# Kernel optimization log

Hardware: AMD Instinct MI355X
Metric: run time of the kernel (lower is better)

Reference implementation:

```python
import jax, jax.numpy as jnp
import numpy as np

AX = (-2, -1)
LAMBDA = 0.05
ITERS = 6

# torch fft_2d_img  = fftshift(ifft2(ifftshift(x)))  (used in the FORWARD model)
# torch ifft_2d_img = ifftshift(fft2(fftshift(x)))   (used in the ADJOINT model)

def _fwd_xform(x):
    return jnp.fft.fftshift(jnp.fft.ifft2(jnp.fft.ifftshift(x, axes=AX), axes=AX, norm='ortho'), axes=AX)

def _adj_xform(x):
    return jnp.fft.ifftshift(jnp.fft.fft2(jnp.fft.fftshift(x, axes=AX), axes=AX, norm='ortho'), axes=AX)

def _forward_model(img, S, mask):
    # img [b,t,h,w] -> masked multicoil k-space [b,t,c,h,w]
    return mask * _fwd_xform(S * img[:, :, None])

def _adjoint_model(k, S):
    # k [b,t,c,h,w] -> coil-combined image [b,t,h,w]
    return jnp.sum(jnp.conj(S) * _adj_xform(k), axis=2)

def _system_matrix_R(p, S, L, mask):
    # p [b,sv,h,w]; L [b,t,sv]
    expanded = jnp.einsum('bts,bshw->bthw', L, p)
    combined = _adjoint_model(_forward_model(expanded, S, mask), S)
    out = jnp.einsum('bts,bthw->bshw', jnp.conj(L), combined)
    return out + LAMBDA * p

def _cg_solve(b_vec, S, L, mask):
    z0 = jnp.zeros_like(b_vec)
    rs0 = jnp.vdot(b_vec, b_vec)

    def step(carry, _):
        z, r, p, rs_old, done = carry
        Ap = _system_matrix_R(p, S, L, mask)
        alpha = rs_old / (jnp.vdot(p, Ap) + 1e-20)
        z_n = z + alpha * p
        r_n = r - alpha * Ap
        rs_new = jnp.vdot(r_n, r_n)
        p_n = r_n + (rs_new / (rs_old + 1e-20)) * p
        # replicate torch early-break: freeze state once residual is tiny
        z_o = jnp.where(done, z, z_n)
        r_o = jnp.where(done, r, r_n)
        p_o = jnp.where(done, p, p_n)
        rs_o = jnp.where(done, rs_old, rs_new)
        done_n = done | (jnp.abs(rs_o) < 1e-10)
        return (z_o, r_o, p_o, rs_o, done_n), None

    carry0 = (z0, b_vec, b_vec, rs0, jnp.array(False))
    (z, _, _, _, _), _ = jax.lax.scan(step, carry0, None, length=ITERS)
    return z

def setup_inputs() -> dict:
    key = jax.random.key(0)
    ks = jax.random.split(key, 9)
    b, t, c, h, w, sv = 2, 12, 10, 256, 256, 3
    f32 = jnp.float32
    inp = {
        'k_real': jax.random.normal(ks[0], (b, t, c, h, w), f32),
        'k_imag': jax.random.normal(ks[1], (b, t, c, h, w), f32),
        'mo_real': jax.random.normal(ks[2], (b, sv, h, w), f32),
        'mo_imag': jax.random.normal(ks[3], (b, sv, h, w), f32),
        's_real': jax.random.normal(ks[4], (b, 1, c, h, w), f32),
        's_imag': jax.random.normal(ks[5], (b, 1, c, h, w), f32),
        'tb_real': jax.random.normal(ks[6], (b, t, sv), f32),
        'tb_imag': jax.random.normal(ks[7], (b, t, sv), f32),
        'mask': (jax.random.uniform(ks[8], (b, t, 1, h, w)) < 0.35).astype(f32),
    }
    return inp

def reference(k_real, k_imag, mo_real, mo_imag, s_real, s_imag, tb_real, tb_imag, mask):
    Y = k_real + 1j * k_imag          # [b,t,c,h,w]
    MO = mo_real + 1j * mo_imag       # [b,sv,h,w]
    S = s_real + 1j * s_imag          # [b,1,c,h,w]
    L = tb_real + 1j * tb_imag        # [b,t,sv]
    # b = L^H A^H Y + lambda * model_output
    b_vec = jnp.einsum('bts,bthw->bshw', jnp.conj(L), _adjoint_model(Y, S)) + LAMBDA * MO
    z = _cg_solve(b_vec, S, L, mask)  # [b,sv,h,w] complex
    return jnp.stack([z.real, z.imag], axis=-1)  # [b,sv,h,w,2] float32
```

## Files before the change

### kernel.cpp

```cpp
#include <hip/hip_runtime.h>
#include <math.h>

#define HW 65536
#define LAM 0.05f

struct Scal {
  double pap_re, pap_im, rq_re, rq_im, qq;
  double rs_old, al_re, al_im, beta;
  int done, apply, cnt, pad;
};

__device__ __forceinline__ float2 cadd(float2 a, float2 b){ return make_float2(a.x+b.x, a.y+b.y); }
__device__ __forceinline__ float2 csub(float2 a, float2 b){ return make_float2(a.x-b.x, a.y-b.y); }
__device__ __forceinline__ float2 cmul(float2 a, float2 b){
  return make_float2(a.x*b.x - a.y*b.y, a.x*b.y + a.y*b.x);
}
__device__ __forceinline__ float2 cmulj(float2 a, float2 b){
  return make_float2(a.x*b.x + a.y*b.y, a.x*b.y - a.y*b.x);
}
__device__ __forceinline__ int swz(int p){ return p ^ (p>>4); }

__device__ __forceinline__ void wave_lds_sync(){
  __builtin_amdgcn_wave_barrier();
  __asm__ __volatile__("s_waitcnt lgkmcnt(0)" ::: "memory");
  __builtin_amdgcn_wave_barrier();
}

template<int S>
__device__ __forceinline__ void bfly4(float2 x0, float2 x1, float2 x2, float2 x3,
                                      float2& y0, float2& y1, float2& y2, float2& y3){
  float2 a  = cadd(x0,x2), bm = csub(x0,x2);
  float2 c  = cadd(x1,x3), d  = csub(x1,x3);
  float2 jd = make_float2(-(float)S*d.y, (float)S*d.x);
  y0 = cadd(a,c); y2 = csub(a,c); y1 = cadd(bm,jd); y3 = csub(bm,jd);
}

template<int S>
__device__ __forceinline__ void dft16(float2* a){
  const float s_ = (float)S;
  const float2 W1 = make_float2( 0.92387953251f,  s_*0.38268343236f);
  const float2 W2 = make_float2( 0.70710678119f,  s_*0.70710678119f);
  const float2 W3 = make_float2( 0.38268343236f,  s_*0.92387953251f);
  const float2 W4_ = make_float2(0.f,              s_*1.f);
  const float2 W6 = make_float2(-0.70710678119f,  s_*0.70710678119f);
  const float2 W9 = make_float2(-0.92387953251f, -s_*0.38268343236f);
  float2 t[16];
#pragma unroll
  for (int n0=0;n0<4;n0++){
    float2 y0,y1,y2,y3;
    bfly4<S>(a[n0], a[n0+4], a[n0+8], a[n0+12], y0,y1,y2,y3);
    if (n0==1){ y1=cmul(y1,W1); y2=cmul(y2,W2); y3=cmul(y3,W3); }
    if (n0==2){ y1=cmul(y1,W2); y2=cmul(y2,W4_); y3=cmul(y3,W6); }
    if (n0==3){ y1=cmul(y1,W3); y2=cmul(y2,W6); y3=cmul(y3,W9); }
    t[n0*4+0]=y0; t[n0*4+1]=y1; t[n0*4+2]=y2; t[n0*4+3]=y3;
  }
#pragma unroll
  for (int k1=0;k1<4;k1++){
    float2 y0,y1,y2,y3;
    bfly4<S>(t[0*4+k1], t[1*4+k1], t[2*4+k1], t[3*4+k1], y0,y1,y2,y3);
    a[k1+0]=y0; a[k1+4]=y1; a[k1+8]=y2; a[k1+12]=y3;
  }
}

template<int S>
__device__ void fft256_r16(float2* buf, int l){
  float2 a[16];
#pragma unroll
  for (int j=0;j<16;j++) a[j] = buf[swz(l + 16*j)];
  dft16<S>(a);
  float ang = (float)S * 6.2831853071795865f * (float)l * (1.f/256.f);
  float sn, cs; __sincosf(ang, &sn, &cs);
  float2 wstep = make_float2(cs, sn);
  float2 w = wstep;
#pragma unroll
  for (int k=1;k<16;k++){ a[k] = cmul(a[k], w); w = cmul(w, wstep); }
#pragma unroll
  for (int k=0;k<16;k++) buf[swz(16*k + l)] = a[k];
  wave_lds_sync();
#pragma unroll
  for (int j=0;j<16;j++) a[j] = buf[swz(16*l + j)];
  dft16<S>(a);
  wave_lds_sync();
#pragma unroll
  for (int k=0;k<16;k++) buf[swz(l + 16*k)] = a[k];
  wave_lds_sync();
}

__global__ __launch_bounds__(256) void k_w(const float* __restrict__ mask,
                                           const float* __restrict__ tbr,
                                           const float* __restrict__ tbi,
                                           float* __restrict__ Wf,
                                           Scal* sc){
  if (blockIdx.x==0 && blockIdx.y==0 && threadIdx.x==0){
    sc->pap_re=0.0; sc->pap_im=0.0; sc->rq_re=0.0; sc->rq_im=0.0; sc->qq=0.0;
    sc->rs_old=0.0; sc->al_re=0.0; sc->al_im=0.0; sc->beta=0.0;
    sc->done=0; sc->apply=0; sc->cnt=0;
  }
  __shared__ float wtf[9][16][17];
  int tid = threadIdx.x;
  int bx = blockIdx.x;
  int b  = blockIdx.y;
  int u0 = (bx>>4)<<4, v0 = (bx&15)<<4;
  int u_l = tid>>4, v_l = tid&15;
  int pix = (u0+u_l)*256 + (v0+v_l);
  float d0=0,d1=0,d2=0, o01r=0,o01i=0, o02r=0,o02i=0, o12r=0,o12i=0;
#pragma unroll
  for (int t=0;t<12;t++){
    float m = mask[(size_t)(b*12+t)*HW + pix];
    int lb = (b*12+t)*3;
    float l0r = tbr[lb+0], l0i = tbi[lb+0];
    float l1r = tbr[lb+1], l1i = tbi[lb+1];
    float l2r = tbr[lb+2], l2i = tbi[lb+2];
    d0 += m*(l0r*l0r + l0i*l0i);
    d1 += m*(l1r*l1r + l1i*l1i);
    d2 += m*(l2r*l2r + l2i*l2i);
    o01r += m*(l0r*l1r + l0i*l1i); o01i += m*(l0r*l1i - l0i*l1r);
    o02r += m*(l0r*l2r + l0i*l2i); o02i += m*(l0r*l2i - l0i*l2r);
    o12r += m*(l1r*l2r + l1i*l2i); o12i += m*(l1r*l2i - l1i*l2r);
  }
  const float s = 1.0f/65536.0f;
  wtf[0][u_l][v_l] = d0*s;   wtf[1][u_l][v_l] = d1*s;   wtf[2][u_l][v_l] = d2*s;
  wtf[3][u_l][v_l] = o01r*s; wtf[4][u_l][v_l] = o01i*s;
  wtf[5][u_l][v_l] = o02r*s; wtf[6][u_l][v_l] = o02i*s;
  wtf[7][u_l][v_l] = o12r*s; wtf[8][u_l][v_l] = o12i*s;
  __syncthreads();
  int u_l2 = tid&15, v_l2 = tid>>4;
#pragma unroll
  for (int f=0;f<9;f++){
    Wf[ ((size_t)(b*9+f)*256 + (v0+v_l2))*256 + (u0+u_l2) ] = wtf[f][u_l2][v_l2];
  }
}

__global__ __launch_bounds__(512) void k_yrow(const float* __restrict__ kr,
                                              const float* __restrict__ ki,
                                              const float* __restrict__ tbr,
                                              const float* __restrict__ tbi,
                                              float2* __restrict__ bufA){
  __shared__ float2 lb[30*257];
  int tid = threadIdx.x;
  int wv = tid>>6, lane = tid&63, g = lane>>4, l = lane&15;
  int px = tid & 255, half = tid >> 8;
  int r = blockIdx.x, b = blockIdx.y;
  float sg = (((r ^ px) & 1) ? -1.f : 1.f) * (1.f/256.f);
  int sk = swz(px);
#pragma unroll
  for (int cc=0; cc<5; cc++){
    int c = half*5 + cc;
    float a0r=0,a0i=0,a1r=0,a1i=0,a2r=0,a2i=0;
#pragma unroll
    for (int t=0;t<12;t++){
      size_t off = ((size_t)((b*12+t)*10+c))*HW + (size_t)r*256 + px;
      float yr = kr[off], yi = ki[off];
      int lbi = (b*12+t)*3;
      float l0r = tbr[lbi+0], l0i = tbi[lbi+0];
      float l1r = tbr[lbi+1], l1i = tbi[lbi+1];
      float l2r = tbr[lbi+2], l2i = tbi[lbi+2];
      a0r += l0r*yr + l0i*yi;  a0i += l0r*yi - l0i*yr;
      a1r += l1r*yr + l1i*yi;  a1i += l1r*yi - l1i*yr;
      a2r += l2r*yr + l2i*yi;  a2i += l2r*yi - l2i*yr;
    }
    lb[(c*3+0)*257 + sk] = make_float2(a0r*sg, a0i*sg);
    lb[(c*3+1)*257 + sk] = make_float2(a1r*sg, a1i*sg);
    lb[(c*3+2)*257 + sk] = make_float2(a2r*sg, a2i*sg);
  }
  __syncthreads();
  int tau = 4*wv + g;
  if (tau < 30){
    float2* lw = &lb[tau*257];
    fft256_r16<-1>(lw, l);
    float2* dst = bufA + (size_t)(b*30+tau)*HW + (size_t)r*256;
#pragma unroll
    for (int j=0;j<8;j++){
      int e = 2*(16*j + l);
      float2 e0 = lw[swz(e)], e1 = lw[swz(e+1)];
      *(float4*)(dst + e) = make_float4(e0.x,e0.y,e1.x,e1.y);
    }
  }
}

template<int MODE>
__global__ __launch_bounds__(384) void k_colpass(float2* __restrict__ bufA,
                                                 const float* __restrict__ Wf){
  __shared__ float2 lb[24*257];
  int tid = threadIdx.x;
  int wv = tid>>6, lane = tid&63, g = lane>>4, l = lane&15;
  int j0 = blockIdx.x*8;
  int c = blockIdx.y, b = blockIdx.z;
#pragma unroll
  for (int it=0; it<8; it++){
    int idx = it*384 + tid;
    int s = idx>>10, rem = idx&1023, u = rem>>2, cp = rem&3;
    const float2* src = bufA + (size_t)(b*30 + c*3 + s)*HW;
    float4 v = *(const float4*)(src + u*256 + j0 + 2*cp);
    lb[(s*8+2*cp  )*257 + swz(u)] = make_float2(v.x, v.y);
    lb[(s*8+2*cp+1)*257 + swz(u)] = make_float2(v.z, v.w);
  }
  __syncthreads();
  int tau = 4*wv + g;
  if (MODE==0){
    fft256_r16<-1>(&lb[tau*257], l);
  } else {
    fft256_r16<1>(&lb[tau*257], l);
    __syncthreads();
    const float* W0 = Wf + (size_t)b*9*HW;
    for (int idx=tid; idx<2048; idx+=384){
      int u = idx&255, col = idx>>8;
      int su = swz(u);
      int v = j0 + col;
      float2 x0 = lb[(0*8+col)*257 + su];
      float2 x1 = lb[(1*8+col)*257 + su];
      float2 x2 = lb[(2*8+col)*257 + su];
      size_t wb = (size_t)v*256 + u;
      float d0  = W0[(size_t)0*HW + wb];
      float d1  = W0[(size_t)1*HW + wb];
      float d2  = W0[(size_t)2*HW + wb];
      float o01r= W0[(size_t)3*HW + wb], o01i = W0[(size_t)4*HW + wb];
      float o02r= W0[(size_t)5*HW + wb], o02i = W0[(size_t)6*HW + wb];
      float o12r= W0[(size_t)7*HW + wb], o12i = W0[(size_t)8*HW + wb];
      float2 y0, y1, y2;
      y0.x = d0*x0.x + o01r*x1.x - o01i*x1.y + o02r*x2.x - o02i*x2.y;
      y0.y = d0*x0.y + o01r*x1.y + o01i*x1.x + o02r*x2.y + o02i*x2.x;
      y1.x = o01r*x0.x + o01i*x0.y + d1*x1.x + o12r*x2.x - o12i*x2.y;
      y1.y = o01r*x0.y - o01i*x0.x + d1*x1.y + o12r*x2.y + o12i*x2.x;
      y2.x = o02r*x0.x + o02i*x0.y + o12r*x1.x + o12i*x1.y + d2*x2.x;
      y2.y = o02r*x0.y - o02i*x0.x + o12r*x1.y - o12i*x1.x + d2*x2.y;
      lb[(0*8+col)*257 + su] = y0;
      lb[(1*8+col)*257 + su] = y1;
      lb[(2*8+col)*257 + su] = y2;
    }
    __syncthreads();
    fft256_r16<-1>(&lb[tau*257], l);
  }
  __syncthreads();
#pragma unroll
  for (int it=0; it<8; it++){
    int idx = it*384 + tid;
    int s = idx>>10, rem = idx&1023, u = rem>>2, cp = rem&3;
    float2* dst = bufA + (size_t)(b*30 + c*3 + s)*HW;
    float2 e0 = lb[(s*8+2*cp  )*257 + swz(u)];
    float2 e1 = lb[(s*8+2*cp+1)*257 + swz(u)];
    *(float4*)(dst + u*256 + j0 + 2*cp) = make_float4(e0.x, e0.y, e1.x, e1.y);
  }
}

__global__ __launch_bounds__(256) void k_combine(const float2* __restrict__ bufA,
                                                 const float* __restrict__ sr_,
                                                 const float* __restrict__ si_,
                                                 const float* __restrict__ mor,
                                                 const float* __restrict__ moi,
                                                 float2* __restrict__ z,
                                                 float2* __restrict__ r,
                                                 float2* __restrict__ p,
                                                 Scal* sc){
  __shared__ double sd[4];
  int tid = threadIdx.x;
  int i = blockIdx.x*256 + tid;
  int pix = i & (HW-1);
  int bs = i >> 16;
  int b = bs/3, s = bs - 3*b;
  float2 acc = make_float2(0.f, 0.f);
#pragma unroll
  for (int c=0;c<10;c++){
    float2 F  = bufA[(size_t)(b*30 + c*3 + s)*HW + pix];
    size_t so = (size_t)(b*10+c)*HW + pix;
    float2 sv = make_float2(sr_[so], si_[so]);
    acc = cadd(acc, cmulj(sv, F));
  }
  float sgl = (((pix>>8)^pix)&1 ? -1.f : 1.f) * LAM;
  acc.x += sgl*mor[i]; acc.y += sgl*moi[i];
  z[i] = make_float2(0.f,0.f);
  r[i] = acc; p[i] = acc;
  double dre = (double)acc.x*acc.x + (double)acc.y*acc.y;
  for (int off=32; off>0; off>>=1) dre += __shfl_down(dre, off, 64);
  if ((tid&63)==0) sd[tid>>6] = dre;
  __syncthreads();
  if (tid==0) atomicAdd(&sc->rs_old, sd[0]+sd[1]+sd[2]+sd[3]);
}

__global__ __launch_bounds__(512) void k_spfft(float2* __restrict__ p,
                                               float2* __restrict__ rvec,
                                               float2* __restrict__ z,
                                               const float2* __restrict__ Ap,
                                               const float* __restrict__ sr_,
                                               const float* __restrict__ si_,
                                               float2* __restrict__ bufA,
                                               Scal* sc){
  __shared__ float2 lb[30*257];
  int tid = threadIdx.x;
  int wv = tid>>6, lane = tid&63, g = lane>>4, l = lane&15;
  int r = blockIdx.x, b = blockIdx.y;
  if (tid < 256){
    int px = tid, sk = swz(px);
    int ap = sc->apply;
    float2 alpha = make_float2((float)sc->al_re, (float)sc->al_im);
    float beta = (float)sc->beta;
    float2 pv[3];
#pragma unroll
    for (int s=0;s<3;s++){
      size_t oi = (size_t)(b*3+s)*HW + (size_t)r*256 + px;
      float2 pvv = p[oi];
      if (ap){
        float2 zv = z[oi], rv = rvec[oi], apv = Ap[oi];
        zv = cadd(zv, cmul(alpha, pvv));
        rv = csub(rv, cmul(alpha, apv));
        float2 pn = make_float2(rv.x + beta*pvv.x, rv.y + beta*pvv.y);
        z[oi] = zv; rvec[oi] = rv; p[oi] = pn;
        pvv = pn;
      }
      pv[s] = pvv;
    }
#pragma unroll
    for (int c=0;c<10;c++){
      size_t so = (size_t)(b*10+c)*HW + (size_t)r*256 + px;
      float2 sv = make_float2(sr_[so], si_[so]);
      lb[(c*3+0)*257 + sk] = cmul(sv, pv[0]);
      lb[(c*3+1)*257 + sk] = cmul(sv, pv[1]);
      lb[(c*3+2)*257 + sk] = cmul(sv, pv[2]);
    }
  }
  __syncthreads();
  int tau = 4*wv + g;
  if (tau < 30){
    float2* lw = &lb[tau*257];
    fft256_r16<1>(lw, l);
    float2* dst = bufA + (size_t)(b*30+tau)*HW + (size_t)r*256;
#pragma unroll
    for (int j=0;j<8;j++){
      int e = 2*(16*j + l);
      float2 e0 = lw[swz(e)], e1 = lw[swz(e+1)];
      *(float4*)(dst + e) = make_float4(e0.x,e0.y,e1.x,e1.y);
    }
  }
}

__global__ __launch_bounds__(512) void k_rowcomb(const float2* __restrict__ bufA,
                                                 const float* __restrict__ sr_,
                                                 const float* __restrict__ si_,
                                                 const float2* __restrict__ pvec,
                                                 const float2* __restrict__ rvec,
                                                 float2* __restrict__ Ap,
                                                 Scal* sc){
  __shared__ float2 lb[30*257];
  __shared__ double sd[5][8];
  int tid = threadIdx.x;
  int wv = tid>>6, lane = tid&63, g = lane>>4, l = lane&15;
  int r = blockIdx.x, b = blockIdx.y;
  int tau = 4*wv + g;
  if (tau < 30){
    const float2* src = bufA + (size_t)(b*30+tau)*HW + (size_t)r*256;
    float2* lw = &lb[tau*257];
#pragma unroll
    for (int j=0;j<8;j++){
      int e = 2*(16*j + l);
      float4 v = *(const float4*)(src + e);
      lw[swz(e)]   = make_float2(v.x, v.y);
      lw[swz(e+1)] = make_float2(v.z, v.w);
    }
    wave_lds_sync();
    fft256_r16<-1>(lw, l);
  }
  __syncthreads();
  double d0=0.0, d1=0.0, d2=0.0, d3=0.0, d4=0.0;
  if (tid < 256){
    int px = tid, sk = swz(px);
    float2 a0={0,0}, a1={0,0}, a2={0,0};
#pragma unroll
    for (int c=0;c<10;c++){
      size_t so = (size_t)(b*10+c)*HW + (size_t)r*256 + px;
      float2 sv = make_float2(sr_[so], si_[so]);
      a0 = cadd(a0, cmulj(sv, lb[(c*3+0)*257 + sk]));
      a1 = cadd(a1, cmulj(sv, lb[(c*3+1)*257 + sk]));
      a2 = cadd(a2, cmulj(sv, lb[(c*3+2)*257 + sk]));
    }
    float2 accs[3] = {a0,a1,a2};
#pragma unroll
    for (int s=0;s<3;s++){
      size_t oi = (size_t)(b*3+s)*HW + (size_t)r*256 + px;
      float2 acc = accs[s];
      float2 av = pvec[oi];
      float2 rv = rvec[oi];
      acc.x += LAM*av.x; acc.y += LAM*av.y;
      Ap[oi] = acc;
      d0 += (double)av.x*acc.x + (double)av.y*acc.y;
      d1 += (double)av.x*acc.y - (double)av.y*acc.x;
      d2 += (double)rv.x*acc.x + (double)rv.y*acc.y;
      d3 += (double)rv.x*acc.y - (double)rv.y*acc.x;
      d4 += (double)acc.x*acc.x + (double)acc.y*acc.y;
    }
  }
  for (int off=32; off>0; off>>=1){
    d0 += __shfl_down(d0, off, 64);
    d1 += __shfl_down(d1, off, 64);
    d2 += __shfl_down(d2, off, 64);
    d3 += __shfl_down(d3, off, 64);
    d4 += __shfl_down(d4, off, 64);
  }
  if (lane==0){ sd[0][wv]=d0; sd[1][wv]=d1; sd[2][wv]=d2; sd[3][wv]=d3; sd[4][wv]=d4; }
  __syncthreads();
  if (tid==0){
    double t0=0,t1=0,t2=0,t3=0,t4=0;
#pragma unroll
    for (int q=0;q<8;q++){ t0+=sd[0][q]; t1+=sd[1][q]; t2+=sd[2][q]; t3+=sd[3][q]; t4+=sd[4][q]; }
    atomicAdd(&sc->pap_re, t0); atomicAdd(&sc->pap_im, t1);
    atomicAdd(&sc->rq_re,  t2); atomicAdd(&sc->rq_im,  t3);
    atomicAdd(&sc->qq,     t4);
    int total = (int)(gridDim.x*gridDim.y);
    int prev = atomicAdd(&sc->cnt, 1);
    if (prev == total-1){
      sc->cnt = 0;
      if (!sc->done){
        double pr = sc->pap_re + 1e-20, pi = sc->pap_im;
        double den = pr*pr + pi*pi;
        double rs = sc->rs_old;
        double alr =  rs*pr/den, ali = -rs*pi/den;
        double rs_new = rs - 2.0*(alr*sc->rq_re - ali*sc->rq_im)
                           + (alr*alr + ali*ali)*sc->qq;
        sc->al_re = alr; sc->al_im = ali;
        sc->beta = rs_new/(rs + 1e-20);
        sc->rs_old = rs_new;
        sc->apply = 1;
        if (fabs(rs_new) < 1e-10) sc->done = 1;
      } else {
        sc->apply = 0;
      }
      sc->pap_re=0.0; sc->pap_im=0.0; sc->rq_re=0.0; sc->rq_im=0.0; sc->qq=0.0;
    }
  }
}

__global__ __launch_bounds__(256) void k_out(const float2* __restrict__ z,
                                             const float2* __restrict__ p,
                                             const Scal* sc,
                                             float* __restrict__ out){
  int i = blockIdx.x*256 + threadIdx.x;
  int pix = i & (HW-1);
  float sgn = (((pix>>8)^pix)&1) ? -1.f : 1.f;
  float2 zv = z[i];
  if (sc->apply){
    float2 alpha = make_float2((float)sc->al_re, (float)sc->al_im);
    zv = cadd(zv, cmul(alpha, p[i]));
  }
  out[2*i]   = sgn*zv.x;
  out[2*i+1] = sgn*zv.y;
}

extern "C" void kernel_launch(void* const* d_in, const int* in_sizes, int n_in,
                              void* d_out, int out_size, void* d_ws, size_t ws_size,
                              hipStream_t stream){
  const float* kr   = (const float*)d_in[0];
  const float* ki   = (const float*)d_in[1];
  const float* mor  = (const float*)d_in[2];
  const float* moi  = (const float*)d_in[3];
  const float* sr   = (const float*)d_in[4];
  const float* si   = (const float*)d_in[5];
  const float* tbr  = (const float*)d_in[6];
  const float* tbi  = (const float*)d_in[7];
  const float* mask = (const float*)d_in[8];
  float* out = (float*)d_out;

  float2* ws   = (float2*)d_ws;
  float2* bufA = ws;
  float*  Wf   = (float*)(ws + 3932160);
  float2* z    = ws + 4521984;
  float2* r    = ws + 4915200;
  float2* p    = ws + 5308416;
  float2* Ap   = ws + 5701632;
  Scal*   sc   = (Scal*)(ws + 6094848);

  k_w<<<dim3(256,2),dim3(256),0,stream>>>(mask, tbr, tbi, Wf, sc);
  k_yrow<<<dim3(256,2),dim3(512),0,stream>>>(kr, ki, tbr, tbi, bufA);
  k_colpass<0><<<dim3(32,10,2),dim3(384),0,stream>>>(bufA, Wf);
  k_combine<<<dim3(1536),dim3(256),0,stream>>>(bufA, sr, si, mor, moi,
                                               z, r, p, sc);
  for (int it=0; it<6; ++it){
    k_spfft<<<dim3(256,2),dim3(512),0,stream>>>(p, r, z, Ap, sr, si, bufA, sc);
    k_colpass<1><<<dim3(32,10,2),dim3(384),0,stream>>>(bufA, Wf);
    k_rowcomb<<<dim3(256,2),dim3(512),0,stream>>>(bufA, sr, si, p, r, Ap, sc);
  }
  k_out<<<dim3(1536),dim3(256),0,stream>>>(z, p, sc, out);
}
```

Baseline: 725.6 us.

## Vectorize loads, interleave weight layout, and spread coil work across all threads

k_yrow now runs 640 threads, one wave per coil, each lane loading float4 of k-space for four pixels. The nine per-pixel weight planes are interleaved into two float4 planes plus one scalar plane, so colpass reads three loads instead of nine. k_spfft and k_rowcomb now use all 512 threads for the coil loops: the p update is staged through shared memory, and the coil sum is split into two halves that are reduced through LDS. The aim is wider memory transactions and less idle half-block time, at the cost of extra LDS traffic and barriers.

```diff
diff --git a/kernel.cpp b/kernel.cpp
--- a/kernel.cpp
+++ b/kernel.cpp
@@ -125,45 +125,64 @@
   wtf[7][u_l][v_l] = o12r*s; wtf[8][u_l][v_l] = o12i*s;
   __syncthreads();
   int u_l2 = tid&15, v_l2 = tid>>4;
-#pragma unroll
-  for (int f=0;f<9;f++){
-    Wf[ ((size_t)(b*9+f)*256 + (v0+v_l2))*256 + (u0+u_l2) ] = wtf[f][u_l2][v_l2];
-  }
-}
-
-__global__ __launch_bounds__(512) void k_yrow(const float* __restrict__ kr,
-                                              const float* __restrict__ ki,
-                                              const float* __restrict__ tbr,
-                                              const float* __restrict__ tbi,
-                                              float2* __restrict__ bufA){
+  float* W0 = Wf + (size_t)b*9*HW;
+  float4* WA = (float4*)W0;
+  float4* WB = (float4*)(W0 + (size_t)4*HW);
+  float*  WC = W0 + (size_t)8*HW;
+  size_t wb = (size_t)(v0+v_l2)*256 + (u0+u_l2);
+  WA[wb] = make_float4(wtf[0][u_l2][v_l2], wtf[1][u_l2][v_l2],
+                       wtf[2][u_l2][v_l2], wtf[3][u_l2][v_l2]);
+  WB[wb] = make_float4(wtf[4][u_l2][v_l2], wtf[5][u_l2][v_l2],
+                       wtf[6][u_l2][v_l2], wtf[7][u_l2][v_l2]);
+  WC[wb] = wtf[8][u_l2][v_l2];
+}
+
+__global__ __launch_bounds__(640,5) void k_yrow(const float* __restrict__ kr,
+                                                const float* __restrict__ ki,
+                                                const float* __restrict__ tbr,
+                                                const float* __restrict__ tbi,
+                                                float2* __restrict__ bufA){
   __shared__ float2 lb[30*257];
   int tid = threadIdx.x;
-  int wv = tid>>6, lane = tid&63, g = lane>>4, l = lane&15;
-  int px = tid & 255, half = tid >> 8;
   int r = blockIdx.x, b = blockIdx.y;
-  float sg = (((r ^ px) & 1) ? -1.f : 1.f) * (1.f/256.f);
-  int sk = swz(px);
-#pragma unroll
-  for (int cc=0; cc<5; cc++){
-    int c = half*5 + cc;
-    float a0r=0,a0i=0,a1r=0,a1i=0,a2r=0,a2i=0;
+  {
+    int c = tid>>6, px4 = tid&63;
+    float ar[3][4], ai[3][4];
+#pragma unroll
+    for (int s=0;s<3;s++)
+#pragma unroll
+      for (int j=0;j<4;j++){ ar[s][j]=0.f; ai[s][j]=0.f; }
 #pragma unroll
     for (int t=0;t<12;t++){
-      size_t off = ((size_t)((b*12+t)*10+c))*HW + (size_t)r*256 + px;
-      float yr = kr[off], yi = ki[off];
+      size_t off = ((size_t)((b*12+t)*10+c))*HW + (size_t)r*256 + 4*px4;
+      float4 yr4 = *(const float4*)(kr + off);
+      float4 yi4 = *(const float4*)(ki + off);
       int lbi = (b*12+t)*3;
       float l0r = tbr[lbi+0], l0i = tbi[lbi+0];
       float l1r = tbr[lbi+1], l1i = tbi[lbi+1];
       float l2r = tbr[lbi+2], l2i = tbi[lbi+2];
-      a0r += l0r*yr + l0i*yi;  a0i += l0r*yi - l0i*yr;
-      a1r += l1r*yr + l1i*yi;  a1i += l1r*yi - l1i*yr;
-      a2r += l2r*yr + l2i*yi;  a2i += l2r*yi - l2i*yr;
-    }
-    lb[(c*3+0)*257 + sk] = make_float2(a0r*sg, a0i*sg);
-    lb[(c*3+1)*257 + sk] = make_float2(a1r*sg, a1i*sg);
-    lb[(c*3+2)*257 + sk] = make_float2(a2r*sg, a2i*sg);
-  }
-  __syncthreads();
+      float yrj[4] = {yr4.x, yr4.y, yr4.z, yr4.w};
+      float yij[4] = {yi4.x, yi4.y, yi4.z, yi4.w};
+#pragma unroll
+      for (int j=0;j<4;j++){
+        float yr = yrj[j], yi = yij[j];
+        ar[0][j] += l0r*yr + l0i*yi;  ai[0][j] += l0r*yi - l0i*yr;
+        ar[1][j] += l1r*yr + l1i*yi;  ai[1][j] += l1r*yi - l1i*yr;
+        ar[2][j] += l2r*yr + l2i*yi;  ai[2][j] += l2r*yi - l2i*yr;
+      }
+    }
+#pragma unroll
+    for (int j=0;j<4;j++){
+      int px = 4*px4 + j;
+      float sg = (((r ^ px) & 1) ? -1.f : 1.f) * (1.f/256.f);
+      int sk = swz(px);
+#pragma unroll
+      for (int s=0;s<3;s++)
+        lb[(c*3+s)*257 + sk] = make_float2(ar[s][j]*sg, ai[s][j]*sg);
+    }
+  }
+  __syncthreads();
+  int wv = tid>>6, lane = tid&63, g = lane>>4, l = lane&15;
   int tau = 4*wv + g;
   if (tau < 30){
     float2* lw = &lb[tau*257];
@@ -203,6 +222,9 @@
     fft256_r16<1>(&lb[tau*257], l);
     __syncthreads();
     const float* W0 = Wf + (size_t)b*9*HW;
+    const float4* WA = (const float4*)W0;
+    const float4* WB = (const float4*)(W0 + (size_t)4*HW);
+    const float*  WC = W0 + (size_t)8*HW;
     for (int idx=tid; idx<2048; idx+=384){
       int u = idx&255, col = idx>>8;
       int su = swz(u);
@@ -211,12 +233,11 @@
       float2 x1 = lb[(1*8+col)*257 + su];
       float2 x2 = lb[(2*8+col)*257 + su];
       size_t wb = (size_t)v*256 + u;
-      float d0  = W0[(size_t)0*HW + wb];
-      float d1  = W0[(size_t)1*HW + wb];
-      float d2  = W0[(size_t)2*HW + wb];
-      float o01r= W0[(size_t)3*HW + wb], o01i = W0[(size_t)4*HW + wb];
-      float o02r= W0[(size_t)5*HW + wb], o02i = W0[(size_t)6*HW + wb];
-      float o12r= W0[(size_t)7*HW + wb], o12i = W0[(size_t)8*HW + wb];
+      float4 wa = WA[wb];
+      float4 wbv = WB[wb];
+      float d0 = wa.x, d1 = wa.y, d2 = wa.z, o01r = wa.w;
+      float o01i = wbv.x, o02r = wbv.y, o02i = wbv.z, o12r = wbv.w;
+      float o12i = WC[wb];
       float2 y0, y1, y2;
       y0.x = d0*x0.x + o01r*x1.x - o01i*x1.y + o02r*x2.x - o02i*x2.y;
       y0.y = d0*x0.y + o01r*x1.y + o01i*x1.x + o02r*x2.y + o02i*x2.x;
@@ -286,36 +307,39 @@
                                                float2* __restrict__ bufA,
                                                Scal* sc){
   __shared__ float2 lb[30*257];
+  __shared__ float2 pbuf[3][256];
   int tid = threadIdx.x;
   int wv = tid>>6, lane = tid&63, g = lane>>4, l = lane&15;
   int r = blockIdx.x, b = blockIdx.y;
-  if (tid < 256){
-    int px = tid, sk = swz(px);
-    int ap = sc->apply;
-    float2 alpha = make_float2((float)sc->al_re, (float)sc->al_im);
-    float beta = (float)sc->beta;
-    float2 pv[3];
-#pragma unroll
-    for (int s=0;s<3;s++){
-      size_t oi = (size_t)(b*3+s)*HW + (size_t)r*256 + px;
-      float2 pvv = p[oi];
-      if (ap){
-        float2 zv = z[oi], rv = rvec[oi], apv = Ap[oi];
-        zv = cadd(zv, cmul(alpha, pvv));
-        rv = csub(rv, cmul(alpha, apv));
-        float2 pn = make_float2(rv.x + beta*pvv.x, rv.y + beta*pvv.y);
-        z[oi] = zv; rvec[oi] = rv; p[oi] = pn;
-        pvv = pn;
-      }
-      pv[s] = pvv;
-    }
-#pragma unroll
-    for (int c=0;c<10;c++){
+  int ap = sc->apply;
+  float2 alpha = make_float2((float)sc->al_re, (float)sc->al_im);
+  float beta = (float)sc->beta;
+  for (int i = tid; i < 768; i += 512){
+    int s = i>>8, px = i&255;
+    size_t oi = (size_t)(b*3+s)*HW + (size_t)r*256 + px;
+    float2 pvv = p[oi];
+    if (ap){
+      float2 zv = z[oi], rv = rvec[oi], apv = Ap[oi];
+      zv = cadd(zv, cmul(alpha, pvv));
+      rv = csub(rv, cmul(alpha, apv));
+      float2 pn = make_float2(rv.x + beta*pvv.x, rv.y + beta*pvv.y);
+      z[oi] = zv; rvec[oi] = rv; p[oi] = pn;
+      pvv = pn;
+    }
+    pbuf[s][px] = pvv;
+  }
+  __syncthreads();
+  {
+    int px = tid & 255, h = tid >> 8, sk = swz(px);
+    float2 pv0 = pbuf[0][px], pv1 = pbuf[1][px], pv2 = pbuf[2][px];
+#pragma unroll
+    for (int k=0;k<5;k++){
+      int c = h + 2*k;
       size_t so = (size_t)(b*10+c)*HW + (size_t)r*256 + px;
       float2 sv = make_float2(sr_[so], si_[so]);
-      lb[(c*3+0)*257 + sk] = cmul(sv, pv[0]);
-      lb[(c*3+1)*257 + sk] = cmul(sv, pv[1]);
-      lb[(c*3+2)*257 + sk] = cmul(sv, pv[2]);
+      lb[(c*3+0)*257 + sk] = cmul(sv, pv0);
+      lb[(c*3+1)*257 + sk] = cmul(sv, pv1);
+      lb[(c*3+2)*257 + sk] = cmul(sv, pv2);
     }
   }
   __syncthreads();
@@ -341,7 +365,8 @@
                                                  float2* __restrict__ Ap,
                                                  Scal* sc){
   __shared__ float2 lb[30*257];
-  __shared__ double sd[5][8];
+  __shared__ float2 part[3][256];
+  __shared__ double sd[5][4];
   int tid = threadIdx.x;
   int wv = tid>>6, lane = tid&63, g = lane>>4, l = lane&15;
   int r = blockIdx.x, b = blockIdx.y;
@@ -360,18 +385,24 @@
     fft256_r16<-1>(lw, l);
   }
   __syncthreads();
+  int px = tid & 255, h = tid >> 8, sk = swz(px);
+  float2 a0={0,0}, a1={0,0}, a2={0,0};
+#pragma unroll
+  for (int k=0;k<5;k++){
+    int c = h + 2*k;
+    size_t so = (size_t)(b*10+c)*HW + (size_t)r*256 + px;
+    float2 sv = make_float2(sr_[so], si_[so]);
+    a0 = cadd(a0, cmulj(sv, lb[(c*3+0)*257 + sk]));
+    a1 = cadd(a1, cmulj(sv, lb[(c*3+1)*257 + sk]));
+    a2 = cadd(a2, cmulj(sv, lb[(c*3+2)*257 + sk]));
+  }
+  if (h==1){ part[0][px]=a0; part[1][px]=a1; part[2][px]=a2; }
+  __syncthreads();
   double d0=0.0, d1=0.0, d2=0.0, d3=0.0, d4=0.0;
   if (tid < 256){
-    int px = tid, sk = swz(px);
-    float2 a0={0,0}, a1={0,0}, a2={0,0};
-#pragma unroll
-    for (int c=0;c<10;c++){
-      size_t so = (size_t)(b*10+c)*HW + (size_t)r*256 + px;
-      float2 sv = make_float2(sr_[so], si_[so]);
-      a0 = cadd(a0, cmulj(sv, lb[(c*3+0)*257 + sk]));
-      a1 = cadd(a1, cmulj(sv, lb[(c*3+1)*257 + sk]));
-      a2 = cadd(a2, cmulj(sv, lb[(c*3+2)*257 + sk]));
-    }
+    a0 = cadd(a0, part[0][px]);
+    a1 = cadd(a1, part[1][px]);
+    a2 = cadd(a2, part[2][px]);
     float2 accs[3] = {a0,a1,a2};
 #pragma unroll
     for (int s=0;s<3;s++){
@@ -395,12 +426,12 @@
     d3 += __shfl_down(d3, off, 64);
     d4 += __shfl_down(d4, off, 64);
   }
-  if (lane==0){ sd[0][wv]=d0; sd[1][wv]=d1; sd[2][wv]=d2; sd[3][wv]=d3; sd[4][wv]=d4; }
+  if (lane==0 && wv<4){ sd[0][wv]=d0; sd[1][wv]=d1; sd[2][wv]=d2; sd[3][wv]=d3; sd[4][wv]=d4; }
   __syncthreads();
   if (tid==0){
     double t0=0,t1=0,t2=0,t3=0,t4=0;
 #pragma unroll
-    for (int q=0;q<8;q++){ t0+=sd[0][q]; t1+=sd[1][q]; t2+=sd[2][q]; t3+=sd[3][q]; t4+=sd[4][q]; }
+    for (int q=0;q<4;q++){ t0+=sd[0][q]; t1+=sd[1][q]; t2+=sd[2][q]; t3+=sd[3][q]; t4+=sd[4][q]; }
     atomicAdd(&sc->pap_re, t0); atomicAdd(&sc->pap_im, t1);
     atomicAdd(&sc->rq_re,  t2); atomicAdd(&sc->rq_im,  t3);
     atomicAdd(&sc->qq,     t4);
@@ -468,7 +499,7 @@
   Scal*   sc   = (Scal*)(ws + 6094848);
 
   k_w<<<dim3(256,2),dim3(256),0,stream>>>(mask, tbr, tbi, Wf, sc);
-  k_yrow<<<dim3(256,2),dim3(512),0,stream>>>(kr, ki, tbr, tbi, bufA);
+  k_yrow<<<dim3(256,2),dim3(640),0,stream>>>(kr, ki, tbr, tbi, bufA);
   k_colpass<0><<<dim3(32,10,2),dim3(384),0,stream>>>(bufA, Wf);
   k_combine<<<dim3(1536),dim3(256),0,stream>>>(bufA, sr, si, mor, moi,
                                                z, r, p, sc);
```

Measured after the change: 751.7 us. 1.04x slower.
